# Kernel optimization log

Measured on AMD Instinct MI355X. Metric: run time of the kernel, lower is better.

## Reference

```python
import jax, jax.numpy as jnp
import numpy as np

NEG_SLOPE = 0.2


def _gat_layer(x, src, dst, W, att_src, att_dst, bias, concat):
    # x: [N, Fin], W: [Fin, H*C], att_*: [H, C], bias: [H*C] or [C]
    N = x.shape[0]
    H, C = att_src.shape
    h = (x @ W).reshape(N, H, C)                      # node features per head
    a_src = jnp.sum(h * att_src, axis=-1)             # [N, H]
    a_dst = jnp.sum(h * att_dst, axis=-1)             # [N, H]
    e = jax.nn.leaky_relu(a_src[src] + a_dst[dst], NEG_SLOPE)  # [E, H]
    # segment softmax over destination nodes
    m = jax.ops.segment_max(e, dst, num_segments=N)   # [N, H]
    m = jnp.where(jnp.isfinite(m), m, 0.0)
    ex = jnp.exp(e - m[dst])
    s = jax.ops.segment_sum(ex, dst, num_segments=N)  # [N, H]
    alpha = ex / (s[dst] + 1e-16)                     # [E, H]
    msg = h[src] * alpha[:, :, None]                  # [E, H, C]
    out = jax.ops.segment_sum(msg, dst, num_segments=N)  # [N, H, C]
    out = out.reshape(N, H * C) if concat else out.mean(axis=1)
    return out + bias


def setup_inputs() -> dict:
    key = jax.random.key(0)
    ks = jax.random.split(key, 20)
    N, E, Fin, Cg, H = 50000, 800000, 128, 64, 4
    HC = H * Cg
    s = 0.1
    x = jax.random.normal(ks[0], (N, Fin), jnp.float32)
    edge_index = jax.random.randint(ks[1], (2, E), 0, N, dtype=jnp.int32)
    inp = {
        'x': x,
        'edge_index': edge_index,
        'W0': jax.random.normal(ks[2], (Fin, HC), jnp.float32) * s,
        'as0': jax.random.normal(ks[3], (H, Cg), jnp.float32) * s,
        'ad0': jax.random.normal(ks[4], (H, Cg), jnp.float32) * s,
        'b0': jnp.zeros((HC,), jnp.float32),
        'W1': jax.random.normal(ks[5], (HC, HC), jnp.float32) * s,
        'as1': jax.random.normal(ks[6], (H, Cg), jnp.float32) * s,
        'ad1': jax.random.normal(ks[7], (H, Cg), jnp.float32) * s,
        'b1': jnp.zeros((HC,), jnp.float32),
        'W2': jax.random.normal(ks[8], (HC, HC), jnp.float32) * s,
        'as2': jax.random.normal(ks[9], (H, Cg), jnp.float32) * s,
        'ad2': jax.random.normal(ks[10], (H, Cg), jnp.float32) * s,
        'b2': jnp.zeros((Cg,), jnp.float32),
        # linear head: 64 -> 128 -> 10
        'lw0': jax.random.normal(ks[11], (Cg, 128), jnp.float32) * s,
        'lb0': jnp.zeros((128,), jnp.float32),
        'lw1': jax.random.normal(ks[12], (128, 10), jnp.float32) * s,
        'lb1': jnp.zeros((10,), jnp.float32),
    }
    return inp


def reference(x, edge_index, W0, as0, ad0, b0, W1, as1, ad1, b1,
              W2, as2, ad2, b2, lw0, lb0, lw1, lb1):
    N = x.shape[0]
    # PyG GATConv add_self_loops=True: append self-loop edges
    loop = jnp.arange(N, dtype=edge_index.dtype)
    src = jnp.concatenate([edge_index[0], loop])
    dst = jnp.concatenate([edge_index[1], loop])
    h = _gat_layer(x, src, dst, W0, as0, ad0, b0, True)
    h = _gat_layer(h, src, dst, W1, as1, ad1, b1, True)
    h = _gat_layer(h, src, dst, W2, as2, ad2, b2, False)
    h = jax.nn.relu(h @ lw0 + lb0)
    return h @ lw1 + lb1
```

## Files before the change

### kernel.cpp

```cpp
#include <hip/hip_runtime.h>
#include <hip/hip_bf16.h>

#define HEADS 4
#define CH 64
#define HC 256

typedef __attribute__((ext_vector_type(8))) short short8;
typedef __attribute__((ext_vector_type(4))) float f32x4;
typedef __attribute__((ext_vector_type(8))) _Float16 half8;

__device__ inline unsigned short f2bf(float f){
  unsigned u = __float_as_uint(f);
  return (unsigned short)((u + 0x7FFF + ((u >> 16) & 1)) >> 16);
}


__global__ void hist_kernel(const int* __restrict__ dst, int E, int ET, int* __restrict__ cnt){
  int e = blockIdx.x * blockDim.x + threadIdx.x;
  if (e >= ET) return;
  int d = (e < E) ? dst[e] : (e - E);
  atomicAdd(&cnt[d], 1);
}

__global__ void blocksum_kernel(const int* __restrict__ cnt, int N, int* __restrict__ bsum){
  int tid = threadIdx.x;
  int i = blockIdx.x * 256 + tid;
  int v = (i < N) ? cnt[i] : 0;
  #pragma unroll
  for (int off = 32; off >= 1; off >>= 1) v += __shfl_xor(v, off);
  __shared__ int ws[4];
  if ((tid & 63) == 0) ws[tid >> 6] = v;
  __syncthreads();
  if (tid == 0) bsum[blockIdx.x] = ws[0] + ws[1] + ws[2] + ws[3];
}

__global__ void scanb_kernel(int* __restrict__ bsum, int nb){
  __shared__ int buf[256];
  int tid = threadIdx.x;
  int v = (tid < nb) ? bsum[tid] : 0;
  buf[tid] = v;
  __syncthreads();
  #pragma unroll
  for (int off = 1; off < 256; off <<= 1){
    int t = (tid >= off) ? buf[tid - off] : 0;
    __syncthreads();
    buf[tid] += t;
    __syncthreads();
  }
  if (tid < nb) bsum[tid] = buf[tid] - v;
}

__global__ void scanfinal_kernel(const int* __restrict__ cnt, const int* __restrict__ bsum,
                                 int* __restrict__ ptr, int* __restrict__ cur, int N){
  __shared__ int buf[256];
  int tid = threadIdx.x;
  int i = blockIdx.x * 256 + tid;
  int v = (i < N) ? cnt[i] : 0;
  buf[tid] = v;
  __syncthreads();
  #pragma unroll
  for (int off = 1; off < 256; off <<= 1){
    int t = (tid >= off) ? buf[tid - off] : 0;
    __syncthreads();
    buf[tid] += t;
    __syncthreads();
  }
  int exc = buf[tid] - v + bsum[blockIdx.x];
  if (i < N){
    ptr[i] = exc; cur[i] = exc;
    if (i == N - 1) ptr[N] = exc + v;
  }
}

__global__ void scatter_kernel(const int* __restrict__ src, const int* __restrict__ dst,
                               int E, int ET, int* __restrict__ cur,
                               int* __restrict__ csr_src, int* __restrict__ csr_dst){
  int e = blockIdx.x * blockDim.x + threadIdx.x;
  if (e >= ET) return;
  int s, d;
  if (e < E){ s = src[e]; d = dst[e]; } else { s = e - E; d = e - E; }
  int pos = atomicAdd(&cur[d], 1);
  csr_src[pos] = s;
  csr_dst[pos] = d;
}


__global__ void ew_kernel(const int* __restrict__ csr_src, const int* __restrict__ csr_dst,
                          const float* __restrict__ a_src, const float* __restrict__ a_dst,
                          float* __restrict__ w, int ET){
  int i = blockIdx.x * 256 + threadIdx.x;
  if (i >= ET) return;
  int s = csr_src[i], d = csr_dst[i];
  float4 as = *(const float4*)&a_src[(size_t)s * 4];
  float4 ad = *(const float4*)&a_dst[(size_t)d * 4];
  float4 r;
  float e;
  e = as.x + ad.x; e = e > 0.f ? e : 0.2f * e; r.x = __expf(e);
  e = as.y + ad.y; e = e > 0.f ? e : 0.2f * e; r.y = __expf(e);
  e = as.z + ad.z; e = e > 0.f ? e : 0.2f * e; r.z = __expf(e);
  e = as.w + ad.w; e = e > 0.f ? e : 0.2f * e; r.w = __expf(e);
  *(float4*)&w[(size_t)i * 4] = r;
}


__global__ void wsplit_kernel(const float* __restrict__ W0, unsigned short* __restrict__ h0,
                              unsigned short* __restrict__ l0,
                              const float* __restrict__ W1, unsigned short* __restrict__ h1,
                              unsigned short* __restrict__ l1,
                              const float* __restrict__ W2, unsigned short* __restrict__ h2,
                              unsigned short* __restrict__ l2){
  int idx = blockIdx.x * 256 + threadIdx.x;
  const float* W; unsigned short *hi, *lo; int K;
  if (idx < 128 * HC){ W = W0; hi = h0; lo = l0; K = 128; }
  else if (idx < (128 + 256) * HC){ idx -= 128 * HC; W = W1; hi = h1; lo = l1; K = 256; }
  else { idx -= (128 + 256) * HC; W = W2; hi = h2; lo = l2; K = 256; }
  int k = idx >> 8, n = idx & 255;
  float w = W[idx];
  unsigned short hb = f2bf(w);
  float hf = __uint_as_float((unsigned)hb << 16);
  unsigned short lb = f2bf(w - hf);
  hi[(size_t)n * K + k] = hb;
  lo[(size_t)n * K + k] = lb;
}


__global__ void xsplit_kernel(const float* __restrict__ x, int total4,
                              unsigned short* __restrict__ xhi, unsigned short* __restrict__ xlo){
  int i4 = blockIdx.x * 256 + threadIdx.x;
  if (i4 >= total4) return;
  float4 v = *(const float4*)&x[(size_t)i4 * 4];
  float va[4] = {v.x, v.y, v.z, v.w};
  unsigned short h4[4], l4[4];
  #pragma unroll
  for (int j = 0; j < 4; j++){
    unsigned short hb = f2bf(va[j]);
    float hf = __uint_as_float((unsigned)hb << 16);
    h4[j] = hb;
    l4[j] = f2bf(va[j] - hf);
  }
  *(ushort4*)&xhi[(size_t)i4 * 4] = make_ushort4(h4[0], h4[1], h4[2], h4[3]);
  *(ushort4*)&xlo[(size_t)i4 * 4] = make_ushort4(l4[0], l4[1], l4[2], l4[3]);
}


__global__ void lwsplit_kernel(const float* __restrict__ lw0,
                               unsigned short* __restrict__ l0hi, unsigned short* __restrict__ l0lo,
                               const float* __restrict__ lw1, _Float16* __restrict__ l1T){
  int idx = blockIdx.x * 256 + threadIdx.x;
  if (idx < 8192){
    int n = idx & 127, k = idx >> 7;
    float w = lw0[k * 128 + n];
    unsigned short hb = f2bf(w);
    float hf = __uint_as_float((unsigned)hb << 16);
    unsigned short lb = f2bf(w - hf);
    l0hi[n * 64 + k] = hb;
    l0lo[n * 64 + k] = lb;
  } else if (idx < 8192 + 2048){
    int id = idx - 8192;
    int n = id & 15, k = id >> 4;
    float w = (n < 10) ? lw1[k * 10 + n] : 0.f;
    l1T[n * 128 + k] = (_Float16)w;
  }
}


__launch_bounds__(256, 2)
__global__ void gemm_mfma_kernel(const unsigned short* __restrict__ Ahi,
                                 const unsigned short* __restrict__ Alo,
                                 const unsigned short* __restrict__ BhiT,
                                 const unsigned short* __restrict__ BloT,
                                 _Float16* __restrict__ Cm,
                                 const float* __restrict__ att_s, const float* __restrict__ att_d,
                                 float* __restrict__ a_src, float* __restrict__ a_dst,
                                 int K){
  __shared__ unsigned short As_hi[128][40];
  __shared__ unsigned short As_lo[128][40];
  __shared__ unsigned short Bs_hi[128][40];
  __shared__ unsigned short Bs_lo[128][40];

  int tid = threadIdx.x;
  int m0 = blockIdx.x * 128, n0 = blockIdx.y * 128;
  int wave = tid >> 6, lane = tid & 63;
  int wm = (wave >> 1) * 64, wn = (wave & 1) * 64;
  int col = lane & 15, quad = lane >> 4;

  f32x4 acc[4][4];
  #pragma unroll
  for (int a = 0; a < 4; a++)
    #pragma unroll
    for (int b = 0; b < 4; b++)
      acc[a][b] = (f32x4){0.f, 0.f, 0.f, 0.f};

  for (int k0 = 0; k0 < K; k0 += 32){
    #pragma unroll
    for (int r = 0; r < 2; r++){
      int id = r * 256 + tid;
      int m = id >> 2, q = id & 3;
      size_t g = (size_t)(m0 + m) * K + k0 + q * 8;
      *(short8*)&As_hi[m][q * 8] = *(const short8*)&Ahi[g];
      *(short8*)&As_lo[m][q * 8] = *(const short8*)&Alo[g];
    }
    #pragma unroll
    for (int r = 0; r < 2; r++){
      int id = r * 256 + tid;
      int n = id >> 2, q = id & 3;
      size_t g = (size_t)(n0 + n) * K + k0 + q * 8;
      *(short8*)&Bs_hi[n][q * 8] = *(const short8*)&BhiT[g];
      *(short8*)&Bs_lo[n][q * 8] = *(const short8*)&BloT[g];
    }
    __syncthreads();

    short8 af[4][2], bf[4][2];
    #pragma unroll
    for (int t = 0; t < 4; t++){
      af[t][0] = *(const short8*)&As_hi[wm + t * 16 + col][quad * 8];
      af[t][1] = *(const short8*)&As_lo[wm + t * 16 + col][quad * 8];
      bf[t][0] = *(const short8*)&Bs_hi[wn + t * 16 + col][quad * 8];
      bf[t][1] = *(const short8*)&Bs_lo[wn + t * 16 + col][quad * 8];
    }
    #pragma unroll
    for (int mt = 0; mt < 4; mt++)
      #pragma unroll
      for (int nt = 0; nt < 4; nt++){
        acc[mt][nt] = __builtin_amdgcn_mfma_f32_16x16x32_bf16(af[mt][0], bf[nt][0], acc[mt][nt], 0, 0, 0);
        acc[mt][nt] = __builtin_amdgcn_mfma_f32_16x16x32_bf16(af[mt][1], bf[nt][0], acc[mt][nt], 0, 0, 0);
        acc[mt][nt] = __builtin_amdgcn_mfma_f32_16x16x32_bf16(af[mt][0], bf[nt][1], acc[mt][nt], 0, 0, 0);
      }
    __syncthreads();
  }

  #pragma unroll
  for (int mt = 0; mt < 4; mt++)
    #pragma unroll
    for (int nt = 0; nt < 4; nt++){
      int colg = n0 + wn + nt * 16 + col;
      #pragma unroll
      for (int r = 0; r < 4; r++){
        int row = m0 + wm + mt * 16 + quad * 4 + r;
        Cm[(size_t)row * HC + colg] = (_Float16)acc[mt][nt][r];
      }
    }

  int head = (n0 + wn) >> 6;
  float asv[4], adv[4];
  #pragma unroll
  for (int nt = 0; nt < 4; nt++){
    asv[nt] = att_s[head * CH + nt * 16 + col];
    adv[nt] = att_d[head * CH + nt * 16 + col];
  }
  #pragma unroll
  for (int mt = 0; mt < 4; mt++){
    float sp[4] = {0.f,0.f,0.f,0.f}, dp[4] = {0.f,0.f,0.f,0.f};
    #pragma unroll
    for (int nt = 0; nt < 4; nt++)
      #pragma unroll
      for (int r = 0; r < 4; r++){
        sp[r] += acc[mt][nt][r] * asv[nt];
        dp[r] += acc[mt][nt][r] * adv[nt];
      }
    #pragma unroll
    for (int off = 1; off <= 8; off <<= 1)
      #pragma unroll
      for (int r = 0; r < 4; r++){
        sp[r] += __shfl_xor(sp[r], off);
        dp[r] += __shfl_xor(dp[r], off);
      }
    if (col == 0){
      #pragma unroll
      for (int r = 0; r < 4; r++){
        int row = m0 + wm + mt * 16 + quad * 4 + r;
        a_src[row * HEADS + head] = sp[r];
        a_dst[row * HEADS + head] = dp[r];
      }
    }
  }
}


__global__ void agg_kernel(const _Float16* __restrict__ h, const float* __restrict__ w,
                           const int* __restrict__ ptr, const int* __restrict__ csr_src,
                           const float* __restrict__ bias,
                           unsigned short* __restrict__ out_hi, unsigned short* __restrict__ out_lo,
                           int N, int mean_mode, const float* __restrict__ b2,
                           float* __restrict__ f2){
  __shared__ float sm[HEADS][CH];
  int n = blockIdx.x;
  int head = threadIdx.x >> 6;
  int lane = threadIdx.x & 63;
  int eg = lane >> 3, c8 = lane & 7;
  int beg = ptr[n], end = ptr[n + 1];

  float acc0[8] = {0.f,0.f,0.f,0.f,0.f,0.f,0.f,0.f};
  float acc1[8] = {0.f,0.f,0.f,0.f,0.f,0.f,0.f,0.f};
  float ss0 = 0.f, ss1 = 0.f;
  int i = beg + eg;
  for (; i + 8 < end; i += 16){
    int s0 = csr_src[i], s1 = csr_src[i + 8];
    float w0 = w[(size_t)i * 4 + head];
    float w1 = w[(size_t)(i + 8) * 4 + head];
    half8 h0 = *(const half8*)&h[(size_t)s0 * HC + head * CH + c8 * 8];
    half8 h1 = *(const half8*)&h[(size_t)s1 * HC + head * CH + c8 * 8];
    #pragma unroll
    for (int j = 0; j < 8; j++){
      acc0[j] += w0 * (float)h0[j];
      acc1[j] += w1 * (float)h1[j];
    }
    ss0 += w0; ss1 += w1;
  }
  if (i < end){
    int s0 = csr_src[i];
    float w0 = w[(size_t)i * 4 + head];
    half8 h0 = *(const half8*)&h[(size_t)s0 * HC + head * CH + c8 * 8];
    #pragma unroll
    for (int j = 0; j < 8; j++) acc0[j] += w0 * (float)h0[j];
    ss0 += w0;
  }
  float ss = ss0 + ss1;
  float acc[8];
  #pragma unroll
  for (int j = 0; j < 8; j++) acc[j] = acc0[j] + acc1[j];
  #pragma unroll
  for (int off = 8; off <= 32; off <<= 1){
    #pragma unroll
    for (int j = 0; j < 8; j++) acc[j] += __shfl_xor(acc[j], off);
    ss += __shfl_xor(ss, off);
  }
  float inv = 1.f / (ss + 1e-16f);
  #pragma unroll
  for (int j = 0; j < 8; j++) acc[j] *= inv;

  if (!mean_mode){
    if (eg == 0){
      const float* bp = &bias[head * CH + c8 * 8];
      short8 hi8, lo8;
      #pragma unroll
      for (int j = 0; j < 8; j++){
        float v = acc[j] + bp[j];
        unsigned short hb = f2bf(v);
        float hf = __uint_as_float((unsigned)hb << 16);
        hi8[j] = (short)hb;
        lo8[j] = (short)f2bf(v - hf);
      }
      size_t o = (size_t)n * HC + head * CH + c8 * 8;
      *(short8*)&out_hi[o] = hi8;
      *(short8*)&out_lo[o] = lo8;
    }
  } else {
    if (eg == 0){
      #pragma unroll
      for (int j = 0; j < 8; j++) sm[head][c8 * 8 + j] = acc[j];
    }
    __syncthreads();
    int t = threadIdx.x;
    if (t < CH)
      f2[(size_t)n * CH + t] =
        0.25f * (sm[0][t] + sm[1][t] + sm[2][t] + sm[3][t]) + b2[t];
  }
}


__launch_bounds__(256, 2)
__global__ void head_mfma_kernel(const float* __restrict__ f2,
                                 const unsigned short* __restrict__ lw0hiT,
                                 const unsigned short* __restrict__ lw0loT,
                                 const _Float16* __restrict__ lw1T,
                                 const float* __restrict__ lb0,
                                 const float* __restrict__ lb1,
                                 float* __restrict__ outp, int N){
  __shared__ __align__(16) unsigned short L[27648];
  __shared__ __align__(16) _Float16 Ls[16][136];
  const int tid = threadIdx.x;
  const int wave = tid >> 6, lane = tid & 63;
  const int col = lane & 15, quad = lane >> 4;
  const int m0 = blockIdx.x * 64;

  { int n = tid >> 4, k = (tid & 15) * 8;
    *(half8*)&Ls[n][k] = *(const half8*)&lw1T[n * 128 + k]; }

  #pragma unroll
  for (int r = 0; r < 2; r++){
    int id = r * 256 + tid;
    int m = id >> 3, q = id & 7;
    int gm = m0 + m;
    float va[8];
    if (gm < N){
      float4 v0 = *(const float4*)&f2[(size_t)gm * CH + q * 8];
      float4 v1 = *(const float4*)&f2[(size_t)gm * CH + q * 8 + 4];
      va[0]=v0.x; va[1]=v0.y; va[2]=v0.z; va[3]=v0.w;
      va[4]=v1.x; va[5]=v1.y; va[6]=v1.z; va[7]=v1.w;
    } else {
      #pragma unroll
      for (int j = 0; j < 8; j++) va[j] = 0.f;
    }
    short8 hi8, lo8;
    #pragma unroll
    for (int j = 0; j < 8; j++){
      unsigned short hb = f2bf(va[j]);
      float hf = __uint_as_float((unsigned)hb << 16);
      hi8[j] = (short)hb;
      lo8[j] = (short)f2bf(va[j] - hf);
    }
    *(short8*)&L[m * 72 + q * 8] = hi8;
    *(short8*)&L[4608 + m * 72 + q * 8] = lo8;
  }
  #pragma unroll
  for (int r = 0; r < 4; r++){
    int id = r * 256 + tid;
    int n = id >> 3, q = id & 7;
    *(short8*)&L[9216 + n * 72 + q * 8]  = *(const short8*)&lw0hiT[n * 64 + q * 8];
    *(short8*)&L[18432 + n * 72 + q * 8] = *(const short8*)&lw0loT[n * 64 + q * 8];
  }
  __syncthreads();

  const int wn = wave * 32;
  f32x4 acc[4][2];
  #pragma unroll
  for (int a = 0; a < 4; a++)
    #pragma unroll
    for (int b = 0; b < 2; b++) acc[a][b] = (f32x4){0.f,0.f,0.f,0.f};

  #pragma unroll
  for (int ks = 0; ks < 2; ks++){
    int k = ks * 32 + quad * 8;
    short8 ah[4], al[4], bh[2], bl[2];
    #pragma unroll
    for (int mt = 0; mt < 4; mt++){
      ah[mt] = *(short8*)&L[(mt * 16 + col) * 72 + k];
      al[mt] = *(short8*)&L[4608 + (mt * 16 + col) * 72 + k];
    }
    #pragma unroll
    for (int nt = 0; nt < 2; nt++){
      bh[nt] = *(short8*)&L[9216 + (wn + nt * 16 + col) * 72 + k];
      bl[nt] = *(short8*)&L[18432 + (wn + nt * 16 + col) * 72 + k];
    }
    #pragma unroll
    for (int mt = 0; mt < 4; mt++)
      #pragma unroll
      for (int nt = 0; nt < 2; nt++){
        acc[mt][nt] = __builtin_amdgcn_mfma_f32_16x16x32_bf16(ah[mt], bh[nt], acc[mt][nt], 0, 0, 0);
        acc[mt][nt] = __builtin_amdgcn_mfma_f32_16x16x32_bf16(al[mt], bh[nt], acc[mt][nt], 0, 0, 0);
        acc[mt][nt] = __builtin_amdgcn_mfma_f32_16x16x32_bf16(ah[mt], bl[nt], acc[mt][nt], 0, 0, 0);
      }
  }
  __syncthreads();

  _Float16* Zp = (_Float16*)L;
  #pragma unroll
  for (int nt = 0; nt < 2; nt++){
    int n = wn + nt * 16 + col;
    float b = lb0[n];
    #pragma unroll
    for (int mt = 0; mt < 4; mt++)
      #pragma unroll
      for (int r2 = 0; r2 < 4; r2++){
        int m = mt * 16 + quad * 4 + r2;
        float z = acc[mt][nt][r2] + b;
        Zp[m * 136 + n] = (_Float16)fmaxf(z, 0.f);
      }
  }
  __syncthreads();

  f32x4 acc2 = (f32x4){0.f,0.f,0.f,0.f};
  #pragma unroll
  for (int ks = 0; ks < 4; ks++){
    int k = ks * 32 + quad * 8;
    half8 a2 = *(half8*)&Zp[(wave * 16 + col) * 136 + k];
    half8 b2v = *(half8*)&Ls[col][k];
    acc2 = __builtin_amdgcn_mfma_f32_16x16x32_f16(a2, b2v, acc2, 0, 0, 0);
  }
  if (col < 10){
    float bb = lb1[col];
    #pragma unroll
    for (int r2 = 0; r2 < 4; r2++){
      int row = m0 + wave * 16 + quad * 4 + r2;
      if (row < N) outp[(size_t)row * 10 + col] = acc2[r2] + bb;
    }
  }
}


extern "C" void kernel_launch(void* const* d_in, const int* in_sizes, int n_in,
                              void* d_out, int out_size, void* d_ws, size_t ws_size,
                              hipStream_t stream) {
  const float* x   = (const float*)d_in[0];
  const int*   ei  = (const int*)d_in[1];
  const float* W0  = (const float*)d_in[2];
  const float* as0 = (const float*)d_in[3];
  const float* ad0 = (const float*)d_in[4];
  const float* b0  = (const float*)d_in[5];
  const float* W1  = (const float*)d_in[6];
  const float* as1 = (const float*)d_in[7];
  const float* ad1 = (const float*)d_in[8];
  const float* b1  = (const float*)d_in[9];
  const float* W2  = (const float*)d_in[10];
  const float* as2 = (const float*)d_in[11];
  const float* ad2 = (const float*)d_in[12];
  const float* b2  = (const float*)d_in[13];
  const float* lw0 = (const float*)d_in[14];
  const float* lb0 = (const float*)d_in[15];
  const float* lw1 = (const float*)d_in[16];
  const float* lb1 = (const float*)d_in[17];
  float* outp = (float*)d_out;

  int N  = in_sizes[0] / 128;
  int E  = in_sizes[1] / 2;
  int ET = E + N;
  int nb = (N + 255) / 256;
  int Mp = ((N + 127) / 128) * 128;

  char* ws = (char*)d_ws;
  _Float16* Hb = (_Float16*)ws;       ws += (size_t)Mp * HC * sizeof(_Float16);
  unsigned short* Fhi = (unsigned short*)ws; ws += (size_t)Mp * HC * 2;
  unsigned short* Flo = (unsigned short*)ws; ws += (size_t)Mp * HC * 2;
  float* f2  = (float*)ws; ws += (size_t)N * CH * sizeof(float);
  float* a_s = (float*)ws; ws += (size_t)Mp * HEADS * sizeof(float);
  float* a_d = (float*)ws; ws += (size_t)Mp * HEADS * sizeof(float);
  float* ewt = (float*)ws; ws += (size_t)ET * HEADS * sizeof(float);
  int* cnt   = (int*)ws;   ws += (size_t)N * sizeof(int);
  int* cur   = (int*)ws;   ws += (size_t)N * sizeof(int);
  int* ptrA  = (int*)ws;   ws += (size_t)(N + 1) * sizeof(int);
  int* bsum  = (int*)ws;   ws += (size_t)nb * sizeof(int);
  int* csr   = (int*)ws;   ws += (size_t)ET * sizeof(int);
  int* csrd  = (int*)ws;   ws += (size_t)ET * sizeof(int);
  unsigned short* w0hi = (unsigned short*)ws; ws += (size_t)128 * HC * 2;
  unsigned short* w0lo = (unsigned short*)ws; ws += (size_t)128 * HC * 2;
  unsigned short* w1hi = (unsigned short*)ws; ws += (size_t)HC * HC * 2;
  unsigned short* w1lo = (unsigned short*)ws; ws += (size_t)HC * HC * 2;
  unsigned short* w2hi = (unsigned short*)ws; ws += (size_t)HC * HC * 2;
  unsigned short* w2lo = (unsigned short*)ws; ws += (size_t)HC * HC * 2;
  unsigned short* l0hi = (unsigned short*)ws; ws += (size_t)8192 * 2;
  unsigned short* l0lo = (unsigned short*)ws; ws += (size_t)8192 * 2;
  _Float16* l1T        = (_Float16*)ws;       ws += (size_t)2048 * 2;

  const int* srcArr = ei;
  const int* dstArr = ei + E;

  hipMemsetAsync(cnt, 0, (size_t)N * sizeof(int), stream);
  hist_kernel<<<(ET + 255) / 256, 256, 0, stream>>>(dstArr, E, ET, cnt);
  blocksum_kernel<<<nb, 256, 0, stream>>>(cnt, N, bsum);
  scanb_kernel<<<1, 256, 0, stream>>>(bsum, nb);
  scanfinal_kernel<<<nb, 256, 0, stream>>>(cnt, bsum, ptrA, cur, N);
  scatter_kernel<<<(ET + 255) / 256, 256, 0, stream>>>(srcArr, dstArr, E, ET, cur, csr, csrd);

  wsplit_kernel<<<((128 + 256 + 256) * HC) / 256, 256, 0, stream>>>(
      W0, w0hi, w0lo, W1, w1hi, w1lo, W2, w2hi, w2lo);
  lwsplit_kernel<<<(8192 + 2048 + 255) / 256, 256, 0, stream>>>(lw0, l0hi, l0lo, lw1, l1T);
  xsplit_kernel<<<(N * 128 / 4 + 255) / 256, 256, 0, stream>>>(x, N * 128 / 4, Fhi, Flo);

  dim3 ggrid(Mp / 128, 2);
  int eb = (ET + 255) / 256;

  gemm_mfma_kernel<<<ggrid, 256, 0, stream>>>(Fhi, Flo, w0hi, w0lo, Hb, as0, ad0, a_s, a_d, 128);
  ew_kernel<<<eb, 256, 0, stream>>>(csr, csrd, a_s, a_d, ewt, ET);
  agg_kernel<<<N, 256, 0, stream>>>(Hb, ewt, ptrA, csr, b0, Fhi, Flo, N, 0, nullptr, nullptr);

  gemm_mfma_kernel<<<ggrid, 256, 0, stream>>>(Fhi, Flo, w1hi, w1lo, Hb, as1, ad1, a_s, a_d, HC);
  ew_kernel<<<eb, 256, 0, stream>>>(csr, csrd, a_s, a_d, ewt, ET);
  agg_kernel<<<N, 256, 0, stream>>>(Hb, ewt, ptrA, csr, b1, Fhi, Flo, N, 0, nullptr, nullptr);

  gemm_mfma_kernel<<<ggrid, 256, 0, stream>>>(Fhi, Flo, w2hi, w2lo, Hb, as2, ad2, a_s, a_d, HC);
  ew_kernel<<<eb, 256, 0, stream>>>(csr, csrd, a_s, a_d, ewt, ET);
  agg_kernel<<<N, 256, 0, stream>>>(Hb, ewt, ptrA, csr, nullptr, nullptr, nullptr, N, 1, b2, f2);

  head_mfma_kernel<<<(N + 63) / 64, 256, 0, stream>>>(f2, l0hi, l0lo, l1T, lb0, lb1, outp, N);
}
```

Measured before the change: 587.9 us.

## Degree-sort nodes and aggregate eight per block; register-prefetch GEMM tiles

```diff
diff --git a/kernel.cpp b/kernel.cpp
--- a/kernel.cpp
+++ b/kernel.cpp
@@ -82,6 +82,37 @@
   int pos = atomicAdd(&cur[d], 1);
   csr_src[pos] = s;
   csr_dst[pos] = d;
+}
+
+
+__global__ void dhist_kernel(const int* __restrict__ cnt, int N, int* __restrict__ dbins){
+  int n = blockIdx.x * 256 + threadIdx.x;
+  if (n >= N) return;
+  int bin = min(cnt[n], 63);
+  atomicAdd(&dbins[bin], 1);
+}
+
+__global__ void dscan_kernel(int* __restrict__ dbins, int* __restrict__ dcur){
+  int lane = threadIdx.x;
+  int v = dbins[lane];
+  int s = v;
+  #pragma unroll
+  for (int off = 1; off < 64; off <<= 1){
+    int t = __shfl_up(s, off);
+    if (lane >= off) s += t;
+  }
+  int exc = s - v;
+  dbins[lane] = exc;
+  dcur[lane] = exc;
+}
+
+__global__ void dscatter_kernel(const int* __restrict__ cnt, int N, int* __restrict__ dcur,
+                                int* __restrict__ perm){
+  int n = blockIdx.x * 256 + threadIdx.x;
+  if (n >= N) return;
+  int bin = min(cnt[n], 63);
+  int pos = atomicAdd(&dcur[bin], 1);
+  perm[pos] = n;
 }
 
 
@@ -184,6 +215,18 @@
   int wm = (wave >> 1) * 64, wn = (wave & 1) * 64;
   int col = lane & 15, quad = lane >> 4;
 
+  int mS = tid >> 2, q8 = (tid & 3) * 8;
+  size_t baseA0 = (size_t)(m0 + mS) * K + q8;
+  size_t baseA1 = (size_t)(m0 + mS + 64) * K + q8;
+  size_t baseB0 = (size_t)(n0 + mS) * K + q8;
+  size_t baseB1 = (size_t)(n0 + mS + 64) * K + q8;
+
+  short8 pA[4], pB[4];
+  pA[0] = *(const short8*)&Ahi[baseA0];  pA[1] = *(const short8*)&Alo[baseA0];
+  pA[2] = *(const short8*)&Ahi[baseA1];  pA[3] = *(const short8*)&Alo[baseA1];
+  pB[0] = *(const short8*)&BhiT[baseB0]; pB[1] = *(const short8*)&BloT[baseB0];
+  pB[2] = *(const short8*)&BhiT[baseB1]; pB[3] = *(const short8*)&BloT[baseB1];
+
   f32x4 acc[4][4];
   #pragma unroll
   for (int a = 0; a < 4; a++)
@@ -192,23 +235,24 @@
       acc[a][b] = (f32x4){0.f, 0.f, 0.f, 0.f};
 
   for (int k0 = 0; k0 < K; k0 += 32){
-    #pragma unroll
-    for (int r = 0; r < 2; r++){
-      int id = r * 256 + tid;
-      int m = id >> 2, q = id & 3;
-      size_t g = (size_t)(m0 + m) * K + k0 + q * 8;
-      *(short8*)&As_hi[m][q * 8] = *(const short8*)&Ahi[g];
-      *(short8*)&As_lo[m][q * 8] = *(const short8*)&Alo[g];
-    }
-    #pragma unroll
-    for (int r = 0; r < 2; r++){
-      int id = r * 256 + tid;
-      int n = id >> 2, q = id & 3;
-      size_t g = (size_t)(n0 + n) * K + k0 + q * 8;
-      *(short8*)&Bs_hi[n][q * 8] = *(const short8*)&BhiT[g];
-      *(short8*)&Bs_lo[n][q * 8] = *(const short8*)&BloT[g];
-    }
     __syncthreads();
+    *(short8*)&As_hi[mS][q8]      = pA[0];
+    *(short8*)&As_lo[mS][q8]      = pA[1];
+    *(short8*)&As_hi[mS + 64][q8] = pA[2];
+    *(short8*)&As_lo[mS + 64][q8] = pA[3];
+    *(short8*)&Bs_hi[mS][q8]      = pB[0];
+    *(short8*)&Bs_lo[mS][q8]      = pB[1];
+    *(short8*)&Bs_hi[mS + 64][q8] = pB[2];
+    *(short8*)&Bs_lo[mS + 64][q8] = pB[3];
+    __syncthreads();
+
+    if (k0 + 32 < K){
+      size_t o = (size_t)(k0 + 32);
+      pA[0] = *(const short8*)&Ahi[baseA0 + o];  pA[1] = *(const short8*)&Alo[baseA0 + o];
+      pA[2] = *(const short8*)&Ahi[baseA1 + o];  pA[3] = *(const short8*)&Alo[baseA1 + o];
+      pB[0] = *(const short8*)&BhiT[baseB0 + o]; pB[1] = *(const short8*)&BloT[baseB0 + o];
+      pB[2] = *(const short8*)&BhiT[baseB1 + o]; pB[3] = *(const short8*)&BloT[baseB1 + o];
+    }
 
     short8 af[4][2], bf[4][2];
     #pragma unroll
@@ -226,7 +270,6 @@
         acc[mt][nt] = __builtin_amdgcn_mfma_f32_16x16x32_bf16(af[mt][1], bf[nt][0], acc[mt][nt], 0, 0, 0);
         acc[mt][nt] = __builtin_amdgcn_mfma_f32_16x16x32_bf16(af[mt][0], bf[nt][1], acc[mt][nt], 0, 0, 0);
       }
-    __syncthreads();
   }
 
   #pragma unroll
@@ -279,58 +322,43 @@
 
 __global__ void agg_kernel(const _Float16* __restrict__ h, const float* __restrict__ w,
                            const int* __restrict__ ptr, const int* __restrict__ csr_src,
+                           const int* __restrict__ perm,
                            const float* __restrict__ bias,
                            unsigned short* __restrict__ out_hi, unsigned short* __restrict__ out_lo,
-                           int N, int mean_mode, const float* __restrict__ b2,
+                           int mean_mode, const float* __restrict__ b2,
                            float* __restrict__ f2){
-  __shared__ float sm[HEADS][CH];
-  int n = blockIdx.x;
+  __shared__ float sm[HEADS][8][CH];
   int head = threadIdx.x >> 6;
   int lane = threadIdx.x & 63;
-  int eg = lane >> 3, c8 = lane & 7;
-  int beg = ptr[n], end = ptr[n + 1];
-
-  float acc0[8] = {0.f,0.f,0.f,0.f,0.f,0.f,0.f,0.f};
-  float acc1[8] = {0.f,0.f,0.f,0.f,0.f,0.f,0.f,0.f};
-  float ss0 = 0.f, ss1 = 0.f;
-  int i = beg + eg;
-  for (; i + 8 < end; i += 16){
-    int s0 = csr_src[i], s1 = csr_src[i + 8];
-    float w0 = w[(size_t)i * 4 + head];
-    float w1 = w[(size_t)(i + 8) * 4 + head];
-    half8 h0 = *(const half8*)&h[(size_t)s0 * HC + head * CH + c8 * 8];
-    half8 h1 = *(const half8*)&h[(size_t)s1 * HC + head * CH + c8 * 8];
-    #pragma unroll
-    for (int j = 0; j < 8; j++){
-      acc0[j] += w0 * (float)h0[j];
-      acc1[j] += w1 * (float)h1[j];
-    }
-    ss0 += w0; ss1 += w1;
-  }
-  if (i < end){
-    int s0 = csr_src[i];
-    float w0 = w[(size_t)i * 4 + head];
-    half8 h0 = *(const half8*)&h[(size_t)s0 * HC + head * CH + c8 * 8];
-    #pragma unroll
-    for (int j = 0; j < 8; j++) acc0[j] += w0 * (float)h0[j];
-    ss0 += w0;
-  }
-  float ss = ss0 + ss1;
-  float acc[8];
-  #pragma unroll
-  for (int j = 0; j < 8; j++) acc[j] = acc0[j] + acc1[j];
-  #pragma unroll
-  for (int off = 8; off <= 32; off <<= 1){
-    #pragma unroll
-    for (int j = 0; j < 8; j++) acc[j] += __shfl_xor(acc[j], off);
-    ss += __shfl_xor(ss, off);
+  int slot = lane >> 3, c8 = lane & 7;
+  int pn = perm[blockIdx.x * 8 + slot];
+  int beg = 0, deg = 0;
+  if (pn >= 0){ beg = ptr[pn]; deg = ptr[pn + 1] - beg; }
+
+  int maxdeg = deg;
+  #pragma unroll
+  for (int off = 8; off <= 32; off <<= 1) maxdeg = max(maxdeg, __shfl_xor(maxdeg, off));
+
+  float acc[8] = {0.f,0.f,0.f,0.f,0.f,0.f,0.f,0.f};
+  float ss = 0.f;
+  #pragma unroll 2
+  for (int it = 0; it < maxdeg; ++it){
+    bool valid = it < deg;
+    int idx = beg + (valid ? it : 0);
+    int s = csr_src[idx];
+    float wv = w[(size_t)idx * 4 + head];
+    wv = valid ? wv : 0.f;
+    half8 hv = *(const half8*)&h[(size_t)s * HC + head * CH + c8 * 8];
+    #pragma unroll
+    for (int j = 0; j < 8; j++) acc[j] += wv * (float)hv[j];
+    ss += wv;
   }
   float inv = 1.f / (ss + 1e-16f);
   #pragma unroll
   for (int j = 0; j < 8; j++) acc[j] *= inv;
 
   if (!mean_mode){
-    if (eg == 0){
+    if (pn >= 0){
       const float* bp = &bias[head * CH + c8 * 8];
       short8 hi8, lo8;
       #pragma unroll
@@ -341,20 +369,21 @@
         hi8[j] = (short)hb;
         lo8[j] = (short)f2bf(v - hf);
       }
-      size_t o = (size_t)n * HC + head * CH + c8 * 8;
+      size_t o = (size_t)pn * HC + head * CH + c8 * 8;
       *(short8*)&out_hi[o] = hi8;
       *(short8*)&out_lo[o] = lo8;
     }
   } else {
-    if (eg == 0){
-      #pragma unroll
-      for (int j = 0; j < 8; j++) sm[head][c8 * 8 + j] = acc[j];
-    }
+    #pragma unroll
+    for (int j = 0; j < 8; j++) sm[head][slot][c8 * 8 + j] = acc[j];
     __syncthreads();
-    int t = threadIdx.x;
-    if (t < CH)
-      f2[(size_t)n * CH + t] =
-        0.25f * (sm[0][t] + sm[1][t] + sm[2][t] + sm[3][t]) + b2[t];
+    for (int t = threadIdx.x; t < 512; t += 256){
+      int sl = t >> 6, ch = t & 63;
+      int pn2 = perm[blockIdx.x * 8 + sl];
+      if (pn2 >= 0)
+        f2[(size_t)pn2 * CH + ch] =
+          0.25f * (sm[0][sl][ch] + sm[1][sl][ch] + sm[2][sl][ch] + sm[3][sl][ch]) + b2[ch];
+    }
   }
 }
 
@@ -507,6 +536,7 @@
   int ET = E + N;
   int nb = (N + 255) / 256;
   int Mp = ((N + 127) / 128) * 128;
+  int Np8 = ((N + 7) / 8) * 8;
 
   char* ws = (char*)d_ws;
   _Float16* Hb = (_Float16*)ws;       ws += (size_t)Mp * HC * sizeof(_Float16);
@@ -522,6 +552,9 @@
   int* bsum  = (int*)ws;   ws += (size_t)nb * sizeof(int);
   int* csr   = (int*)ws;   ws += (size_t)ET * sizeof(int);
   int* csrd  = (int*)ws;   ws += (size_t)ET * sizeof(int);
+  int* perm  = (int*)ws;   ws += (size_t)Np8 * sizeof(int);
+  int* dbins = (int*)ws;   ws += 64 * sizeof(int);
+  int* dcur  = (int*)ws;   ws += 64 * sizeof(int);
   unsigned short* w0hi = (unsigned short*)ws; ws += (size_t)128 * HC * 2;
   unsigned short* w0lo = (unsigned short*)ws; ws += (size_t)128 * HC * 2;
   unsigned short* w1hi = (unsigned short*)ws; ws += (size_t)HC * HC * 2;
@@ -536,12 +569,18 @@
   const int* dstArr = ei + E;
 
   hipMemsetAsync(cnt, 0, (size_t)N * sizeof(int), stream);
+  hipMemsetAsync(dbins, 0, 64 * sizeof(int), stream);
+  hipMemsetAsync(perm, 0xFF, (size_t)Np8 * sizeof(int), stream);
   hist_kernel<<<(ET + 255) / 256, 256, 0, stream>>>(dstArr, E, ET, cnt);
   blocksum_kernel<<<nb, 256, 0, stream>>>(cnt, N, bsum);
   scanb_kernel<<<1, 256, 0, stream>>>(bsum, nb);
   scanfinal_kernel<<<nb, 256, 0, stream>>>(cnt, bsum, ptrA, cur, N);
   scatter_kernel<<<(ET + 255) / 256, 256, 0, stream>>>(srcArr, dstArr, E, ET, cur, csr, csrd);
 
+  dhist_kernel<<<nb, 256, 0, stream>>>(cnt, N, dbins);
+  dscan_kernel<<<1, 64, 0, stream>>>(dbins, dcur);
+  dscatter_kernel<<<nb, 256, 0, stream>>>(cnt, N, dcur, perm);
+
   wsplit_kernel<<<((128 + 256 + 256) * HC) / 256, 256, 0, stream>>>(
       W0, w0hi, w0lo, W1, w1hi, w1lo, W2, w2hi, w2lo);
   lwsplit_kernel<<<(8192 + 2048 + 255) / 256, 256, 0, stream>>>(lw0, l0hi, l0lo, lw1, l1T);
@@ -549,18 +588,19 @@
 
   dim3 ggrid(Mp / 128, 2);
   int eb = (ET + 255) / 256;
+  int ab = Np8 / 8;
 
   gemm_mfma_kernel<<<ggrid, 256, 0, stream>>>(Fhi, Flo, w0hi, w0lo, Hb, as0, ad0, a_s, a_d, 128);
   ew_kernel<<<eb, 256, 0, stream>>>(csr, csrd, a_s, a_d, ewt, ET);
-  agg_kernel<<<N, 256, 0, stream>>>(Hb, ewt, ptrA, csr, b0, Fhi, Flo, N, 0, nullptr, nullptr);
+  agg_kernel<<<ab, 256, 0, stream>>>(Hb, ewt, ptrA, csr, perm, b0, Fhi, Flo, 0, nullptr, nullptr);
 
   gemm_mfma_kernel<<<ggrid, 256, 0, stream>>>(Fhi, Flo, w1hi, w1lo, Hb, as1, ad1, a_s, a_d, HC);
   ew_kernel<<<eb, 256, 0, stream>>>(csr, csrd, a_s, a_d, ewt, ET);
-  agg_kernel<<<N, 256, 0, stream>>>(Hb, ewt, ptrA, csr, b1, Fhi, Flo, N, 0, nullptr, nullptr);
+  agg_kernel<<<ab, 256, 0, stream>>>(Hb, ewt, ptrA, csr, perm, b1, Fhi, Flo, 0, nullptr, nullptr);
 
   gemm_mfma_kernel<<<ggrid, 256, 0, stream>>>(Fhi, Flo, w2hi, w2lo, Hb, as2, ad2, a_s, a_d, HC);
   ew_kernel<<<eb, 256, 0, stream>>>(csr, csrd, a_s, a_d, ewt, ET);
-  agg_kernel<<<N, 256, 0, stream>>>(Hb, ewt, ptrA, csr, nullptr, nullptr, nullptr, N, 1, b2, f2);
+  agg_kernel<<<ab, 256, 0, stream>>>(Hb, ewt, ptrA, csr, perm, nullptr, nullptr, nullptr, 1, b2, f2);
 
   head_mfma_kernel<<<(N + 63) / 64, 256, 0, stream>>>(f2, l0hi, l0lo, l1T, lb0, lb1, outp, N);
 }
```

New measurement: 861.5 us. 46.5% more time.
